# Optimization experiments

Measured on AMD Instinct MI355X. Metric: run time of the kernel, lower is better.

Reference implementation:

```python
import jax, jax.numpy as jnp
import numpy as np

BT = 64  # chunk size

def _l2norm(x, eps=1e-6):
    n = jnp.linalg.norm(x, axis=-1, keepdims=True)
    return x / jnp.maximum(n, eps)

def _kda_gate(g_raw, A_log, dt_bias):
    # g = -exp(A_log) * softplus(g_raw + dt_bias); broadcast A_log over K
    return -jnp.exp(A_log)[None, None, :, None] * jax.nn.softplus(g_raw.astype(jnp.float32) + dt_bias[None, None].astype(jnp.float32))

def _chunk_kda_fwd(q, k, v, g, beta):
    B, T, H, K = q.shape
    V = v.shape[-1]
    assert T % BT == 0
    NT = T // BT
    scale = K ** -0.5
    q = _l2norm(q.astype(jnp.float32)) * scale
    k = _l2norm(k.astype(jnp.float32))

    def to_chunks(x, d):
        # [B,T,H,d] -> [NT,B,H,BT,d]
        return x.astype(jnp.float32).transpose(0, 2, 1, 3).reshape(B, H, NT, BT, d).transpose(2, 0, 1, 3, 4)

    qc, kc, vc, gc = to_chunks(q, K), to_chunks(k, K), to_chunks(v, V), to_chunks(g, K)
    bc = beta.astype(jnp.float32).transpose(0, 2, 1).reshape(B, H, NT, BT).transpose(2, 0, 1, 3)  # [NT,B,H,BT]

    eye = jnp.eye(BT, dtype=jnp.float32)
    tril_strict = jnp.tril(jnp.ones((BT, BT), bool), -1)
    tril_incl = jnp.tril(jnp.ones((BT, BT), bool), 0)

    def body(S, xs):
        q_i, k_i, v_i, g_i, b_i = xs  # [B,H,BT,*]
        gcum = jnp.cumsum(g_i, axis=-2)                              # [B,H,BT,K]
        diff = gcum[:, :, :, None, :] - gcum[:, :, None, :, :]      # [B,H,BT,BT,K]
        decay = jnp.exp(jnp.minimum(diff, 0.0))
        # intra-chunk k-k matrix, beta row-scaled, strictly lower, negated
        Akk = jnp.einsum('bhik,bhjk,bhijk->bhij', k_i, k_i, decay)
        M = -jnp.where(tril_strict, Akk * b_i[..., :, None], 0.0)
        # UT transform: torch in-place loop solves Tm = (I - M)^{-1}
        Tm = jax.scipy.linalg.solve_triangular(eye - M, jnp.broadcast_to(eye, M.shape), lower=True)
        Afin = Tm * b_i[..., None, :]                                # column scale by beta
        k_eg = k_i * jnp.exp(gcum)
        w = Afin @ k_eg                                              # [B,H,BT,K]
        u = Afin @ v_i                                               # [B,H,BT,V]
        Aqk = jnp.einsum('bhik,bhjk,bhijk->bhij', q_i, k_i, decay)
        Aqk = jnp.where(tril_incl, Aqk, 0.0)
        v_new = u - w @ S
        o_i = (q_i * jnp.exp(gcum)) @ S + Aqk @ v_new
        g_last = gcum[:, :, -1, :]                                   # [B,H,K]
        k_dec = jnp.exp(g_last[:, :, None, :] - gcum) * k_i
        S_new = S * jnp.exp(g_last)[..., None] + jnp.einsum('bhck,bhcv->bhkv', k_dec, v_new)
        return S_new, o_i

    S0 = jnp.zeros((B, H, K, V), jnp.float32)
    _, o = jax.lax.scan(body, S0, (qc, kc, vc, gc, bc))              # o: [NT,B,H,BT,V]
    return o.transpose(1, 2, 0, 3, 4).reshape(B, H, T, V).transpose(0, 2, 1, 3)


def setup_inputs() -> dict:
    key = jax.random.key(0)
    ks = jax.random.split(key, 7)
    B, T, H, K, V = 2, 8192, 16, 32, 64
    return {
        'q': jax.random.normal(ks[0], (B, T, H, K), jnp.float32),
        'k': jax.random.normal(ks[1], (B, T, H, K), jnp.float32),
        'v': jax.random.normal(ks[2], (B, T, H, V), jnp.float32),
        'g_raw': jax.random.normal(ks[3], (B, T, H, K), jnp.float32),
        'beta': jax.random.uniform(ks[4], (B, T, H), jnp.float32),
        'A_log': jax.random.normal(ks[5], (H,), jnp.float32) - 3.0,  # moderate decay rate
        'dt_bias': jax.random.normal(ks[6], (H, K), jnp.float32) * 0.1,
    }


def reference(q, k, v, g_raw, beta, A_log, dt_bias):
    g = _kda_gate(g_raw, A_log, dt_bias)
    return _chunk_kda_fwd(q, k, v, g, beta)
```

## Files before the change

### kernel.cpp

```cpp
#include <hip/hip_runtime.h>
#include <math.h>

#define Tt 8192
#define Hh 16
#define NCH 4096

#define OFF_U   ((size_t)NCH*2048)
#define OFF_M   ((size_t)NCH*6144)
#define OFF_C   ((size_t)NCH*7168)
#define OFF_MS  ((size_t)NCH*9216)
#define OFF_CS  (OFF_MS + (size_t)256*1024)
#define OFF_SS  (OFF_CS + (size_t)256*2048)

__device__ __forceinline__ float softplusf(float x) {
  return fmaxf(x, 0.f) + log1pf(__expf(-fabsf(x)));
}

__global__ __launch_bounds__(256) void kda_phase1(
    const float* __restrict__ kin, const float* __restrict__ vin,
    const float* __restrict__ graw, const float* __restrict__ beta,
    const float* __restrict__ A_log, const float* __restrict__ dt_bias,
    float* __restrict__ ws)
{
  __shared__ float sG[64*33];
  __shared__ float sK[64*33];
  __shared__ float sL[64*64];
  __shared__ float sT[64*65];
  __shared__ float sC2[3*272];
  __shared__ float sEgl[32];

  const int tid = threadIdx.x;
  const int ch = blockIdx.x;
  const int c = ch >> 5, bh = ch & 31;
  const int b = bh >> 4, h = bh & 15;
  const int t0 = c*64;
  const int iq = tid >> 2, kq = (tid & 3)*8;

  float* wsW = ws;
  float* wsU = ws + OFF_U;
  float* wsM = ws + OFF_M;
  float* wsCc= ws + OFF_C;

  const float negA = -__expf(A_log[h]);

  {
    const float* gr = graw + (((size_t)b*Tt + t0 + iq)*Hh + h)*32 + kq;
    const float* db = dt_bias + h*32 + kq;
    #pragma unroll
    for (int r = 0; r < 8; ++r)
      sG[iq*33 + kq + r] = negA * softplusf(gr[r] + db[r]);
  }
  __syncthreads();
  if (tid < 32) {
    float acc = 0.f;
    for (int i = 0; i < 64; ++i) { acc += sG[i*33 + tid]; sG[i*33 + tid] = acc; }
  }
  {
    const float* kp = kin + (((size_t)b*Tt + t0 + iq)*Hh + h)*32 + kq;
    float kr[8]; float ss = 0.f;
    #pragma unroll
    for (int r = 0; r < 8; ++r) { kr[r] = kp[r]; ss += kr[r]*kr[r]; }
    ss += __shfl_xor(ss, 1); ss += __shfl_xor(ss, 2);
    const float sc = 1.f / fmaxf(sqrtf(ss), 1e-6f);
    #pragma unroll
    for (int r = 0; r < 8; ++r) sK[iq*33 + kq + r] = kr[r]*sc;
  }
  __syncthreads();

  const float b_cm = beta[((size_t)b*Tt + t0 + (tid & 63))*Hh + h];
  float* P  = sT;
  float* Qb = sT + 2112;
  const int i64 = tid & 63, jj2 = (tid >> 6)*2;
  for (int jt = 0; jt < 8; ++jt) {
    const int j0 = jt*8;
    #pragma unroll
    for (int r = 0; r < 8; ++r) {
      const int idx = iq*33 + kq + r;
      P[idx] = sK[idx] * __expf(fminf(sG[idx] - sG[j0*33 + kq + r], 0.f));
    }
    {
      const int jj = tid >> 5, kk = tid & 31;
      Qb[jj*32 + kk] = sK[(j0+jj)*33 + kk] * __expf(sG[j0*33 + kk] - sG[(j0+jj)*33 + kk]);
    }
    __syncthreads();
    float a0 = 0.f, a1 = 0.f;
    #pragma unroll
    for (int hf = 0; hf < 2; ++hf) {
      const int k0 = hf*16;
      float qa[16], qb[16];
      #pragma unroll
      for (int t4 = 0; t4 < 4; ++t4) {
        float4 xa = *(const float4*)(Qb + (jj2  )*32 + k0 + t4*4);
        float4 xb = *(const float4*)(Qb + (jj2+1)*32 + k0 + t4*4);
        qa[t4*4+0]=xa.x; qa[t4*4+1]=xa.y; qa[t4*4+2]=xa.z; qa[t4*4+3]=xa.w;
        qb[t4*4+0]=xb.x; qb[t4*4+1]=xb.y; qb[t4*4+2]=xb.z; qb[t4*4+3]=xb.w;
      }
      #pragma unroll
      for (int kk = 0; kk < 16; ++kk) {
        const float p = P[i64*33 + k0 + kk];
        a0 += p * qa[kk]; a1 += p * qb[kk];
      }
    }
    const int j_0 = j0 + jj2;
    sL[(j_0  )*64 + i64] = (i64 > j_0  ) ? a0*b_cm : 0.f;
    sL[(j_0+1)*64 + i64] = (i64 > j_0+1) ? a1*b_cm : 0.f;
    __syncthreads();
  }

  for (int e = tid; e < 4096; e += 256) {
    const int row = e >> 6, col = e & 63;
    sT[row*65 + col] = (row == col) ? 1.f : 0.f;
  }
  __syncthreads();
  if (tid < 64) {
    const int p = tid >> 4, col = tid & 15;
    for (int i = 1; i < 16; ++i) {
      const int gi = p*16 + i, gc = p*16 + col;
      float acc = 0.f;
      for (int j = 0; j < i; ++j)
        acc -= sL[(p*16+j)*64 + gi] * sT[(p*16+j)*65 + gc];
      sT[gi*65 + gc] = acc + ((i == col) ? 1.f : 0.f);
    }
  }
  __syncthreads();
  {
    const int wid = tid >> 6;
    const int lane = tid & 63;
    const int ri = lane & 15, c4 = (lane >> 4)*4;
    auto offblk = [&](int p, int q) {
      float a0=0.f, a1=0.f, a2=0.f, a3=0.f;
      for (int m = q; m < p; ++m) {
        #pragma unroll
        for (int j = 0; j < 16; ++j) {
          const float lv = sL[(m*16+j)*64 + p*16+ri];
          const float* tp = sT + (m*16+j)*65 + q*16 + c4;
          a0 += lv*tp[0]; a1 += lv*tp[1]; a2 += lv*tp[2]; a3 += lv*tp[3];
        }
      }
      float* cp = sC2 + wid*272 + ri*17 + c4;
      cp[0]=a0; cp[1]=a1; cp[2]=a2; cp[3]=a3;
      float b0=0.f, b1=0.f, b2=0.f, b3=0.f;
      #pragma unroll
      for (int j = 0; j < 16; ++j) {
        const float tv = sT[(p*16+ri)*65 + p*16 + j];
        const float* cj = sC2 + wid*272 + j*17 + c4;
        b0 += tv*cj[0]; b1 += tv*cj[1]; b2 += tv*cj[2]; b3 += tv*cj[3];
      }
      float* op = sT + (p*16+ri)*65 + q*16 + c4;
      op[0]=-b0; op[1]=-b1; op[2]=-b2; op[3]=-b3;
    };
    if (wid == 0) offblk(1,0); else if (wid == 1) offblk(2,1); else if (wid == 2) offblk(3,2);
    __syncthreads();
    if (wid == 0) offblk(2,0); else if (wid == 1) offblk(3,1);
    __syncthreads();
    if (wid == 0) offblk(3,0);
  }
  __syncthreads();

  {
    const float b_row = beta[((size_t)b*Tt + t0 + iq)*Hh + h];
    #pragma unroll
    for (int r = 0; r < 8; ++r) {
      const int idx = iq*33 + kq + r;
      const float g = sG[idx], kn = sK[idx];
      sL[iq*32 + kq + r] = b_row * kn * __expf(g);
      sK[idx] = kn * __expf(sG[63*33 + kq + r] - g);
    }
    if (tid < 32) sEgl[tid] = __expf(sG[63*33 + tid]);
  }
  __syncthreads();

  {
    float acc[8] = {0,0,0,0,0,0,0,0};
    for (int j = 0; j <= iq; ++j) {
      const float t = sT[iq*65 + j];
      const float4 e0 = *(const float4*)(sL + j*32 + kq);
      const float4 e1 = *(const float4*)(sL + j*32 + kq + 4);
      acc[0]+=t*e0.x; acc[1]+=t*e0.y; acc[2]+=t*e0.z; acc[3]+=t*e0.w;
      acc[4]+=t*e1.x; acc[5]+=t*e1.y; acc[6]+=t*e1.z; acc[7]+=t*e1.w;
    }
    #pragma unroll
    for (int r = 0; r < 8; ++r) {
      wsW[(size_t)ch*2048 + tid*8 + r] = acc[r];
      sG[iq*32 + kq + r] = acc[r];
    }
  }
  __syncthreads();

  {
    #pragma unroll
    for (int r = 0; r < 4; ++r) {
      const int f = tid + 256*r;
      const int j = f >> 4, qd = f & 15;
      const float bj = beta[((size_t)b*Tt + t0 + j)*Hh + h];
      float4 v4 = *(const float4*)(vin + (((size_t)b*Tt + t0 + j)*Hh + h)*64 + qd*4);
      v4.x *= bj; v4.y *= bj; v4.z *= bj; v4.w *= bj;
      *(float4*)(sL + j*64 + qd*4) = v4;
    }
  }
  __syncthreads();

  float uacc[16];
  {
    const int vs = (tid & 3)*16;
    #pragma unroll
    for (int r = 0; r < 16; ++r) uacc[r] = 0.f;
    for (int j = 0; j <= iq; ++j) {
      const float t = sT[iq*65 + j];
      const float4 e0 = *(const float4*)(sL + j*64 + vs);
      const float4 e1 = *(const float4*)(sL + j*64 + vs + 4);
      const float4 e2 = *(const float4*)(sL + j*64 + vs + 8);
      const float4 e3 = *(const float4*)(sL + j*64 + vs + 12);
      uacc[0]+=t*e0.x;  uacc[1]+=t*e0.y;  uacc[2]+=t*e0.z;  uacc[3]+=t*e0.w;
      uacc[4]+=t*e1.x;  uacc[5]+=t*e1.y;  uacc[6]+=t*e1.z;  uacc[7]+=t*e1.w;
      uacc[8]+=t*e2.x;  uacc[9]+=t*e2.y;  uacc[10]+=t*e2.z; uacc[11]+=t*e2.w;
      uacc[12]+=t*e3.x; uacc[13]+=t*e3.y; uacc[14]+=t*e3.z; uacc[15]+=t*e3.w;
    }
    #pragma unroll
    for (int rr = 0; rr < 4; ++rr) {
      float4 o4; o4.x=uacc[rr*4]; o4.y=uacc[rr*4+1]; o4.z=uacc[rr*4+2]; o4.w=uacc[rr*4+3];
      *(float4*)(wsU + (size_t)ch*4096 + tid*16 + rr*4) = o4;
    }
  }
  __syncthreads();
  {
    const int vs = (tid & 3)*16;
    #pragma unroll
    for (int rr = 0; rr < 4; ++rr) {
      float4 o4; o4.x=uacc[rr*4]; o4.y=uacc[rr*4+1]; o4.z=uacc[rr*4+2]; o4.w=uacc[rr*4+3];
      *(float4*)(sL + iq*64 + vs + rr*4) = o4;
    }
  }
  __syncthreads();

  {
    const int a = tid >> 3, b4 = (tid & 7)*4, v8 = (tid & 7)*8;
    float mA[4] = {0,0,0,0};
    float cA[8] = {0,0,0,0,0,0,0,0};
    for (int t = 0; t < 64; ++t) {
      const float kd = sK[t*33 + a];
      const float4 wv = *(const float4*)(sG + t*32 + b4);
      mA[0]+=kd*wv.x; mA[1]+=kd*wv.y; mA[2]+=kd*wv.z; mA[3]+=kd*wv.w;
      const float4 u0 = *(const float4*)(sL + t*64 + v8);
      const float4 u1 = *(const float4*)(sL + t*64 + v8 + 4);
      cA[0]+=kd*u0.x; cA[1]+=kd*u0.y; cA[2]+=kd*u0.z; cA[3]+=kd*u0.w;
      cA[4]+=kd*u1.x; cA[5]+=kd*u1.y; cA[6]+=kd*u1.z; cA[7]+=kd*u1.w;
    }
    float4 m4;
    m4.x = ((a == b4+0) ? sEgl[a] : 0.f) - mA[0];
    m4.y = ((a == b4+1) ? sEgl[a] : 0.f) - mA[1];
    m4.z = ((a == b4+2) ? sEgl[a] : 0.f) - mA[2];
    m4.w = ((a == b4+3) ? sEgl[a] : 0.f) - mA[3];
    *(float4*)(wsM + (size_t)ch*1024 + tid*4) = m4;
    float4 c0, c1;
    c0.x=cA[0]; c0.y=cA[1]; c0.z=cA[2]; c0.w=cA[3];
    c1.x=cA[4]; c1.y=cA[5]; c1.z=cA[6]; c1.w=cA[7];
    *(float4*)(wsCc + (size_t)ch*2048 + tid*8) = c0;
    *(float4*)(wsCc + (size_t)ch*2048 + tid*8 + 4) = c1;
  }
}

__global__ __launch_bounds__(256) void kda_scanA(float* __restrict__ ws)
{
  __shared__ float sMa[32*33];
  __shared__ float sMc[32*33];
  __shared__ float sCa[32*18];
  const int tid = threadIdx.x;
  const int vt = blockIdx.x & 3, seg = (blockIdx.x >> 2) & 7, bh = blockIdx.x >> 5;
  const int v0 = vt*16;
  const int a = tid >> 3, b4 = (tid & 7)*4, c2 = (tid & 7)*2;
  const float* wsM = ws + OFF_M;
  const float* wsC = ws + OFF_C;

  #pragma unroll
  for (int r = 0; r < 4; ++r) sMa[a*33 + b4 + r] = (a == b4 + r) ? 1.f : 0.f;
  sCa[a*18 + c2] = 0.f; sCa[a*18 + c2 + 1] = 0.f;
  __syncthreads();

  for (int i = 0; i < 16; ++i) {
    const int ch = (seg*16 + i)*32 + bh;
    float4 m4 = *(const float4*)(wsM + (size_t)ch*1024 + tid*4);
    float2 cc = *(const float2*)(wsC + (size_t)ch*2048 + a*64 + v0 + c2);
    sMc[a*33+b4+0]=m4.x; sMc[a*33+b4+1]=m4.y; sMc[a*33+b4+2]=m4.z; sMc[a*33+b4+3]=m4.w;
    __syncthreads();
    float cn0 = cc.x, cn1 = cc.y;
    float mn0=0.f, mn1=0.f, mn2=0.f, mn3=0.f;
    for (int bb = 0; bb < 32; ++bb) {
      const float m = sMc[a*33 + bb];
      const float2 s2 = *(const float2*)(sCa + bb*18 + c2);
      cn0 += m*s2.x; cn1 += m*s2.y;
      mn0 += m*sMa[bb*33+b4+0]; mn1 += m*sMa[bb*33+b4+1];
      mn2 += m*sMa[bb*33+b4+2]; mn3 += m*sMa[bb*33+b4+3];
    }
    __syncthreads();
    sCa[a*18+c2] = cn0; sCa[a*18+c2+1] = cn1;
    sMa[a*33+b4+0]=mn0; sMa[a*33+b4+1]=mn1; sMa[a*33+b4+2]=mn2; sMa[a*33+b4+3]=mn3;
    __syncthreads();
  }
  const size_t sid = (size_t)(bh*8 + seg);
  float* wsMs = ws + OFF_MS;
  float* wsCs = ws + OFF_CS;
  if (vt == 0) {
    #pragma unroll
    for (int r = 0; r < 4; ++r) wsMs[sid*1024 + tid*4 + r] = sMa[a*33+b4+r];
  }
  float2 co; co.x = sCa[a*18+c2]; co.y = sCa[a*18+c2+1];
  *(float2*)(wsCs + sid*2048 + a*64 + v0 + c2) = co;
}

__global__ __launch_bounds__(256) void kda_scanB(float* __restrict__ ws)
{
  __shared__ float sS[32*64];
  __shared__ float sM[32*33];
  __shared__ float sC2[32*64];
  const int tid = threadIdx.x;
  const int bh = blockIdx.x;
  const int a = tid >> 3, b4 = (tid & 7)*4, v8 = (tid & 7)*8;
  const float* wsMs = ws + OFF_MS;
  const float* wsCs = ws + OFF_CS;
  float* wsSs = ws + OFF_SS;

  #pragma unroll
  for (int r = 0; r < 8; ++r) sS[a*64 + v8 + r] = 0.f;
  __syncthreads();
  for (int seg = 0; seg < 8; ++seg) {
    const size_t sid = (size_t)(bh*8 + seg);
    #pragma unroll
    for (int r = 0; r < 8; ++r) wsSs[sid*2048 + tid*8 + r] = sS[a*64+v8+r];
    float4 m4 = *(const float4*)(wsMs + sid*1024 + tid*4);
    float4 c0 = *(const float4*)(wsCs + sid*2048 + tid*8);
    float4 c1 = *(const float4*)(wsCs + sid*2048 + tid*8 + 4);
    sM[a*33+b4+0]=m4.x; sM[a*33+b4+1]=m4.y; sM[a*33+b4+2]=m4.z; sM[a*33+b4+3]=m4.w;
    sC2[a*64+v8+0]=c0.x; sC2[a*64+v8+1]=c0.y; sC2[a*64+v8+2]=c0.z; sC2[a*64+v8+3]=c0.w;
    sC2[a*64+v8+4]=c1.x; sC2[a*64+v8+5]=c1.y; sC2[a*64+v8+6]=c1.z; sC2[a*64+v8+7]=c1.w;
    __syncthreads();
    float n0=0,n1=0,n2=0,n3=0,n4=0,n5=0,n6=0,n7=0;
    for (int bb = 0; bb < 32; ++bb) {
      const float m = sM[a*33 + bb];
      const float4 s0 = *(const float4*)(sS + bb*64 + v8);
      const float4 s1 = *(const float4*)(sS + bb*64 + v8 + 4);
      n0 += m*s0.x; n1 += m*s0.y; n2 += m*s0.z; n3 += m*s0.w;
      n4 += m*s1.x; n5 += m*s1.y; n6 += m*s1.z; n7 += m*s1.w;
    }
    n0 += sC2[a*64+v8+0]; n1 += sC2[a*64+v8+1]; n2 += sC2[a*64+v8+2]; n3 += sC2[a*64+v8+3];
    n4 += sC2[a*64+v8+4]; n5 += sC2[a*64+v8+5]; n6 += sC2[a*64+v8+6]; n7 += sC2[a*64+v8+7];
    __syncthreads();
    sS[a*64+v8+0]=n0; sS[a*64+v8+1]=n1; sS[a*64+v8+2]=n2; sS[a*64+v8+3]=n3;
    sS[a*64+v8+4]=n4; sS[a*64+v8+5]=n5; sS[a*64+v8+6]=n6; sS[a*64+v8+7]=n7;
    __syncthreads();
  }
}

__global__ __launch_bounds__(256) void kda_scanC(float* __restrict__ ws)
{
  __shared__ float sM[32*33];
  __shared__ float sS[32*18];
  const int tid = threadIdx.x;
  const int vt = blockIdx.x & 3, seg = (blockIdx.x >> 2) & 7, bh = blockIdx.x >> 5;
  const int v0 = vt*16;
  const int a = tid >> 3, b4 = (tid & 7)*4, c2 = (tid & 7)*2;
  const float* wsM = ws + OFF_M;
  float* wsC = ws + OFF_C;
  const float* wsSs = ws + OFF_SS;

  const size_t sid = (size_t)(bh*8 + seg);
  {
    float2 s0 = *(const float2*)(wsSs + sid*2048 + a*64 + v0 + c2);
    sS[a*18 + c2] = s0.x; sS[a*18 + c2 + 1] = s0.y;
  }
  __syncthreads();

  for (int i = 0; i < 16; ++i) {
    const int ch = (seg*16 + i)*32 + bh;
    float4 m4 = *(const float4*)(wsM + (size_t)ch*1024 + tid*4);
    float2 cc = *(const float2*)(wsC + (size_t)ch*2048 + a*64 + v0 + c2);
    sM[a*33+b4+0]=m4.x; sM[a*33+b4+1]=m4.y; sM[a*33+b4+2]=m4.z; sM[a*33+b4+3]=m4.w;
    float2 se; se.x = sS[a*18+c2]; se.y = sS[a*18+c2+1];
    *(float2*)(wsC + (size_t)ch*2048 + a*64 + v0 + c2) = se;
    __syncthreads();
    float n0 = cc.x, n1 = cc.y;
    for (int bb = 0; bb < 32; ++bb) {
      const float m = sM[a*33 + bb];
      const float2 s2 = *(const float2*)(sS + bb*18 + c2);
      n0 += m*s2.x; n1 += m*s2.y;
    }
    __syncthreads();
    sS[a*18+c2] = n0; sS[a*18+c2+1] = n1;
    __syncthreads();
  }
}

__global__ __launch_bounds__(256) void kda_phase3(
    const float* __restrict__ qin, const float* __restrict__ kin,
    const float* __restrict__ graw,
    const float* __restrict__ A_log, const float* __restrict__ dt_bias,
    const float* __restrict__ ws, float* __restrict__ out)
{
  __shared__ float sG[64*33];
  __shared__ float sQ[64*33];
  __shared__ float sA[64*65];
  __shared__ float sV[64*64];

  const int tid = threadIdx.x;
  const int ch = blockIdx.x;
  const int c = ch >> 5, bh = ch & 31;
  const int b = bh >> 4, h = bh & 15;
  const int t0 = c*64;
  const int iq = tid >> 2, kq = (tid & 3)*8;

  const float* wsW = ws;
  const float* wsU = ws + OFF_U;
  const float* wsS = ws + OFF_C;

  const float negA = -__expf(A_log[h]);
  {
    const float* gr = graw + (((size_t)b*Tt + t0 + iq)*Hh + h)*32 + kq;
    const float* db = dt_bias + h*32 + kq;
    #pragma unroll
    for (int r = 0; r < 8; ++r)
      sG[iq*33 + kq + r] = negA * softplusf(gr[r] + db[r]);
  }
  __syncthreads();
  if (tid < 32) {
    float acc = 0.f;
    for (int i = 0; i < 64; ++i) { acc += sG[i*33 + tid]; sG[i*33 + tid] = acc; }
  }
  float knr[8];
  {
    const float* qp = qin + (((size_t)b*Tt + t0 + iq)*Hh + h)*32 + kq;
    float qr[8]; float ssq = 0.f;
    #pragma unroll
    for (int r = 0; r < 8; ++r) { qr[r] = qp[r]; ssq += qr[r]*qr[r]; }
    ssq += __shfl_xor(ssq, 1); ssq += __shfl_xor(ssq, 2);
    const float scq = 0.17677669529663687f / fmaxf(sqrtf(ssq), 1e-6f);
    #pragma unroll
    for (int r = 0; r < 8; ++r) sQ[iq*33 + kq + r] = qr[r]*scq;

    const float* kp = kin + (((size_t)b*Tt + t0 + iq)*Hh + h)*32 + kq;
    float ssk = 0.f;
    #pragma unroll
    for (int r = 0; r < 8; ++r) { knr[r] = kp[r]; ssk += knr[r]*knr[r]; }
    ssk += __shfl_xor(ssk, 1); ssk += __shfl_xor(ssk, 2);
    const float sck = 1.f / fmaxf(sqrtf(ssk), 1e-6f);
    #pragma unroll
    for (int r = 0; r < 8; ++r) knr[r] *= sck;
  }
  __syncthreads();

  float* P  = sV;
  float* Qb = sV + 2112;
  const int i64 = tid & 63, jj2 = (tid >> 6)*2;
  for (int jt = 0; jt < 8; ++jt) {
    const int j0 = jt*8;
    #pragma unroll
    for (int r = 0; r < 8; ++r) {
      const int idx = iq*33 + kq + r;
      P[idx] = sQ[idx] * __expf(fminf(sG[idx] - sG[j0*33 + kq + r], 0.f));
    }
    if (iq >= j0 && iq < j0 + 8) {
      const int jj = iq - j0;
      #pragma unroll
      for (int r = 0; r < 8; ++r)
        Qb[jj*32 + kq + r] = knr[r] * __expf(sG[j0*33 + kq + r] - sG[iq*33 + kq + r]);
    }
    __syncthreads();
    float a0 = 0.f, a1 = 0.f;
    #pragma unroll
    for (int hf = 0; hf < 2; ++hf) {
      const int k0 = hf*16;
      float qa[16], qb[16];
      #pragma unroll
      for (int t4 = 0; t4 < 4; ++t4) {
        float4 xa = *(const float4*)(Qb + (jj2  )*32 + k0 + t4*4);
        float4 xb = *(const float4*)(Qb + (jj2+1)*32 + k0 + t4*4);
        qa[t4*4+0]=xa.x; qa[t4*4+1]=xa.y; qa[t4*4+2]=xa.z; qa[t4*4+3]=xa.w;
        qb[t4*4+0]=xb.x; qb[t4*4+1]=xb.y; qb[t4*4+2]=xb.z; qb[t4*4+3]=xb.w;
      }
      #pragma unroll
      for (int kk = 0; kk < 16; ++kk) {
        const float p = P[i64*33 + k0 + kk];
        a0 += p * qa[kk]; a1 += p * qb[kk];
      }
    }
    const int j_0 = j0 + jj2;
    sA[i64*65 + j_0  ] = (i64 >= j_0  ) ? a0 : 0.f;
    sA[i64*65 + j_0+1] = (i64 >= j_0+1) ? a1 : 0.f;
    __syncthreads();
  }

  float qgr[8];
  {
    #pragma unroll
    for (int r = 0; r < 8; ++r) {
      const int idx = iq*33 + kq + r;
      qgr[r] = sQ[idx] * __expf(sG[idx]);
    }
  }
  __syncthreads();
  {
    #pragma unroll
    for (int rr = 0; rr < 2; ++rr) {
      const int f = tid + 256*rr;
      *(float4*)(sG + f*4) = *(const float4*)(wsS + (size_t)ch*2048 + f*4);
    }
    *(float4*)(sV + tid*8)     = *(const float4*)(wsW + (size_t)ch*2048 + tid*8);
    *(float4*)(sV + tid*8 + 4) = *(const float4*)(wsW + (size_t)ch*2048 + tid*8 + 4);
  }
  __syncthreads();
  {
    float qe[8];
    #pragma unroll
    for (int r = 0; r < 8; ++r) qe[r] = qgr[r];
    for (int j = 0; j <= iq; ++j) {
      const float av = sA[iq*65 + j];
      const float4 w0 = *(const float4*)(sV + j*32 + kq);
      const float4 w1 = *(const float4*)(sV + j*32 + kq + 4);
      qe[0]-=av*w0.x; qe[1]-=av*w0.y; qe[2]-=av*w0.z; qe[3]-=av*w0.w;
      qe[4]-=av*w1.x; qe[5]-=av*w1.y; qe[6]-=av*w1.z; qe[7]-=av*w1.w;
    }
    #pragma unroll
    for (int r = 0; r < 8; ++r) sQ[iq*33 + kq + r] = qe[r];
  }
  __syncthreads();
  {
    #pragma unroll
    for (int rr = 0; rr < 4; ++rr) {
      const int f = tid + 256*rr;
      *(float4*)(sV + f*4) = *(const float4*)(wsU + (size_t)ch*4096 + f*4);
    }
  }
  __syncthreads();
  {
    const int vs = (tid & 3)*16;
    float acc[16];
    #pragma unroll
    for (int r = 0; r < 16; ++r) acc[r] = 0.f;
    for (int kk = 0; kk < 32; ++kk) {
      const float qv = sQ[iq*33 + kk];
      const float4 s0 = *(const float4*)(sG + kk*64 + vs);
      const float4 s1 = *(const float4*)(sG + kk*64 + vs + 4);
      const float4 s2 = *(const float4*)(sG + kk*64 + vs + 8);
      const float4 s3 = *(const float4*)(sG + kk*64 + vs + 12);
      acc[0]+=qv*s0.x;  acc[1]+=qv*s0.y;  acc[2]+=qv*s0.z;  acc[3]+=qv*s0.w;
      acc[4]+=qv*s1.x;  acc[5]+=qv*s1.y;  acc[6]+=qv*s1.z;  acc[7]+=qv*s1.w;
      acc[8]+=qv*s2.x;  acc[9]+=qv*s2.y;  acc[10]+=qv*s2.z; acc[11]+=qv*s2.w;
      acc[12]+=qv*s3.x; acc[13]+=qv*s3.y; acc[14]+=qv*s3.z; acc[15]+=qv*s3.w;
    }
    for (int j = 0; j <= iq; ++j) {
      const float av = sA[iq*65 + j];
      const float4 u0 = *(const float4*)(sV + j*64 + vs);
      const float4 u1 = *(const float4*)(sV + j*64 + vs + 4);
      const float4 u2 = *(const float4*)(sV + j*64 + vs + 8);
      const float4 u3 = *(const float4*)(sV + j*64 + vs + 12);
      acc[0]+=av*u0.x;  acc[1]+=av*u0.y;  acc[2]+=av*u0.z;  acc[3]+=av*u0.w;
      acc[4]+=av*u1.x;  acc[5]+=av*u1.y;  acc[6]+=av*u1.z;  acc[7]+=av*u1.w;
      acc[8]+=av*u2.x;  acc[9]+=av*u2.y;  acc[10]+=av*u2.z; acc[11]+=av*u2.w;
      acc[12]+=av*u3.x; acc[13]+=av*u3.y; acc[14]+=av*u3.z; acc[15]+=av*u3.w;
    }
    float* op = out + (((size_t)b*Tt + t0 + iq)*Hh + h)*64 + vs;
    #pragma unroll
    for (int rr = 0; rr < 4; ++rr) {
      float4 o4; o4.x=acc[rr*4]; o4.y=acc[rr*4+1]; o4.z=acc[rr*4+2]; o4.w=acc[rr*4+3];
      *(float4*)(op + rr*4) = o4;
    }
  }
}

extern "C" void kernel_launch(void* const* d_in, const int* in_sizes, int n_in,
                              void* d_out, int out_size, void* d_ws, size_t ws_size,
                              hipStream_t stream) {
  const float* q    = (const float*)d_in[0];
  const float* k    = (const float*)d_in[1];
  const float* v    = (const float*)d_in[2];
  const float* graw = (const float*)d_in[3];
  const float* beta = (const float*)d_in[4];
  const float* A_log= (const float*)d_in[5];
  const float* dtb  = (const float*)d_in[6];
  float* out = (float*)d_out;
  float* ws  = (float*)d_ws;

  kda_phase1<<<NCH, 256, 0, stream>>>(k, v, graw, beta, A_log, dtb, ws);
  kda_scanA<<<1024, 256, 0, stream>>>(ws);
  kda_scanB<<<32, 256, 0, stream>>>(ws);
  kda_scanC<<<1024, 256, 0, stream>>>(ws);
  kda_phase3<<<NCH, 256, 0, stream>>>(q, k, graw, A_log, dtb, ws, out);
}
```

Measured before the change: 572.6 us.

## Double block size for chunk kernels, split scanB over V, prefetch scan loads

Phase1 and phase3 move from 256 to 512 threads per chunk, so each thread handles 4 K-elements instead of 8. The intra-chunk loops, the block-triangular inverse (now two 256-thread groups) and the state-update products are re-indexed to match. scanB is split across V tiles to run on 128 blocks instead of 32. scanA, scanB and scanC now prefetch the next chunk's M/C from global memory and drop one barrier per iteration. The aim is more parallelism and latency hiding, at the cost of more barriers per thread and heavier per-block shared-memory occupancy.

```diff
diff --git a/kernel.cpp b/kernel.cpp
--- a/kernel.cpp
+++ b/kernel.cpp
@@ -16,7 +16,7 @@
   return fmaxf(x, 0.f) + log1pf(__expf(-fabsf(x)));
 }
 
-__global__ __launch_bounds__(256) void kda_phase1(
+__global__ __launch_bounds__(512, 6) void kda_phase1(
     const float* __restrict__ kin, const float* __restrict__ vin,
     const float* __restrict__ graw, const float* __restrict__ beta,
     const float* __restrict__ A_log, const float* __restrict__ dt_bias,
@@ -26,7 +26,7 @@
   __shared__ float sK[64*33];
   __shared__ float sL[64*64];
   __shared__ float sT[64*65];
-  __shared__ float sC2[3*272];
+  __shared__ float sC2[2*272];
   __shared__ float sEgl[32];
 
   const int tid = threadIdx.x;
@@ -34,7 +34,7 @@
   const int c = ch >> 5, bh = ch & 31;
   const int b = bh >> 4, h = bh & 15;
   const int t0 = c*64;
-  const int iq = tid >> 2, kq = (tid & 3)*8;
+  const int iq = tid >> 3, kq = (tid & 7)*4;
 
   float* wsW = ws;
   float* wsU = ws + OFF_U;
@@ -47,23 +47,29 @@
     const float* gr = graw + (((size_t)b*Tt + t0 + iq)*Hh + h)*32 + kq;
     const float* db = dt_bias + h*32 + kq;
     #pragma unroll
-    for (int r = 0; r < 8; ++r)
+    for (int r = 0; r < 4; ++r)
       sG[iq*33 + kq + r] = negA * softplusf(gr[r] + db[r]);
   }
   __syncthreads();
   if (tid < 32) {
-    float acc = 0.f;
-    for (int i = 0; i < 64; ++i) { acc += sG[i*33 + tid]; sG[i*33 + tid] = acc; }
+    float c0 = 0.f;
+    for (int blk = 0; blk < 4; ++blk) {
+      float v[16];
+      #pragma unroll
+      for (int i = 0; i < 16; ++i) v[i] = sG[(blk*16+i)*33 + tid];
+      #pragma unroll
+      for (int i = 0; i < 16; ++i) { c0 += v[i]; sG[(blk*16+i)*33 + tid] = c0; }
+    }
   }
   {
     const float* kp = kin + (((size_t)b*Tt + t0 + iq)*Hh + h)*32 + kq;
-    float kr[8]; float ss = 0.f;
-    #pragma unroll
-    for (int r = 0; r < 8; ++r) { kr[r] = kp[r]; ss += kr[r]*kr[r]; }
-    ss += __shfl_xor(ss, 1); ss += __shfl_xor(ss, 2);
+    float kr[4]; float ss = 0.f;
+    #pragma unroll
+    for (int r = 0; r < 4; ++r) { kr[r] = kp[r]; ss += kr[r]*kr[r]; }
+    ss += __shfl_xor(ss, 1); ss += __shfl_xor(ss, 2); ss += __shfl_xor(ss, 4);
     const float sc = 1.f / fmaxf(sqrtf(ss), 1e-6f);
     #pragma unroll
-    for (int r = 0; r < 8; ++r) sK[iq*33 + kq + r] = kr[r]*sc;
+    for (int r = 0; r < 4; ++r) sK[iq*33 + kq + r] = kr[r]*sc;
   }
   __syncthreads();
 
@@ -71,10 +77,10 @@
   float* P  = sT;
   float* Qb = sT + 2112;
   const int i64 = tid & 63, jj2 = (tid >> 6)*2;
-  for (int jt = 0; jt < 8; ++jt) {
-    const int j0 = jt*8;
-    #pragma unroll
-    for (int r = 0; r < 8; ++r) {
+  for (int jt = 0; jt < 4; ++jt) {
+    const int j0 = jt*16;
+    #pragma unroll
+    for (int r = 0; r < 4; ++r) {
       const int idx = iq*33 + kq + r;
       P[idx] = sK[idx] * __expf(fminf(sG[idx] - sG[j0*33 + kq + r], 0.f));
     }
@@ -84,19 +90,18 @@
     }
     __syncthreads();
     float a0 = 0.f, a1 = 0.f;
-    #pragma unroll
-    for (int hf = 0; hf < 2; ++hf) {
-      const int k0 = hf*16;
-      float qa[16], qb[16];
-      #pragma unroll
-      for (int t4 = 0; t4 < 4; ++t4) {
+    for (int k8 = 0; k8 < 4; ++k8) {
+      const int k0 = k8*8;
+      float qa[8], qb[8];
+      #pragma unroll
+      for (int t4 = 0; t4 < 2; ++t4) {
         float4 xa = *(const float4*)(Qb + (jj2  )*32 + k0 + t4*4);
         float4 xb = *(const float4*)(Qb + (jj2+1)*32 + k0 + t4*4);
         qa[t4*4+0]=xa.x; qa[t4*4+1]=xa.y; qa[t4*4+2]=xa.z; qa[t4*4+3]=xa.w;
         qb[t4*4+0]=xb.x; qb[t4*4+1]=xb.y; qb[t4*4+2]=xb.z; qb[t4*4+3]=xb.w;
       }
       #pragma unroll
-      for (int kk = 0; kk < 16; ++kk) {
+      for (int kk = 0; kk < 8; ++kk) {
         const float p = P[i64*33 + k0 + kk];
         a0 += p * qa[kk]; a1 += p * qb[kk];
       }
@@ -107,7 +112,7 @@
     __syncthreads();
   }
 
-  for (int e = tid; e < 4096; e += 256) {
+  for (int e = tid; e < 4096; e += 512) {
     const int row = e >> 6, col = e & 63;
     sT[row*65 + col] = (row == col) ? 1.f : 0.f;
   }
@@ -124,43 +129,36 @@
   }
   __syncthreads();
   {
-    const int wid = tid >> 6;
-    const int lane = tid & 63;
-    const int ri = lane & 15, c4 = (lane >> 4)*4;
-    auto offblk = [&](int p, int q) {
-      float a0=0.f, a1=0.f, a2=0.f, a3=0.f;
+    const int grp = tid >> 8, gl = tid & 255;
+    const int ri = gl & 15, cc = gl >> 4;
+    auto offblk1 = [&](int p, int q) {
+      float acc = 0.f;
       for (int m = q; m < p; ++m) {
         #pragma unroll
-        for (int j = 0; j < 16; ++j) {
-          const float lv = sL[(m*16+j)*64 + p*16+ri];
-          const float* tp = sT + (m*16+j)*65 + q*16 + c4;
-          a0 += lv*tp[0]; a1 += lv*tp[1]; a2 += lv*tp[2]; a3 += lv*tp[3];
-        }
+        for (int j = 0; j < 16; ++j)
+          acc += sL[(m*16+j)*64 + p*16+ri] * sT[(m*16+j)*65 + q*16+cc];
       }
-      float* cp = sC2 + wid*272 + ri*17 + c4;
-      cp[0]=a0; cp[1]=a1; cp[2]=a2; cp[3]=a3;
-      float b0=0.f, b1=0.f, b2=0.f, b3=0.f;
-      #pragma unroll
-      for (int j = 0; j < 16; ++j) {
-        const float tv = sT[(p*16+ri)*65 + p*16 + j];
-        const float* cj = sC2 + wid*272 + j*17 + c4;
-        b0 += tv*cj[0]; b1 += tv*cj[1]; b2 += tv*cj[2]; b3 += tv*cj[3];
-      }
-      float* op = sT + (p*16+ri)*65 + q*16 + c4;
-      op[0]=-b0; op[1]=-b1; op[2]=-b2; op[3]=-b3;
+      sC2[grp*272 + ri*17 + cc] = acc;
     };
-    if (wid == 0) offblk(1,0); else if (wid == 1) offblk(2,1); else if (wid == 2) offblk(3,2);
-    __syncthreads();
-    if (wid == 0) offblk(2,0); else if (wid == 1) offblk(3,1);
-    __syncthreads();
-    if (wid == 0) offblk(3,0);
-  }
-  __syncthreads();
+    auto offblk2 = [&](int p, int q) {
+      float bacc = 0.f;
+      #pragma unroll
+      for (int j = 0; j < 16; ++j)
+        bacc += sT[(p*16+ri)*65 + p*16 + j] * sC2[grp*272 + j*17 + cc];
+      sT[(p*16+ri)*65 + q*16+cc] = -bacc;
+    };
+    int p = grp ? 2 : 1, q = grp ? 1 : 0;
+    offblk1(p,q); __syncthreads(); offblk2(p,q); __syncthreads();
+    p = grp ? 3 : 2; q = grp ? 2 : 0;
+    offblk1(p,q); __syncthreads(); offblk2(p,q); __syncthreads();
+    p = 3; q = grp ? 1 : 0;
+    offblk1(p,q); __syncthreads(); offblk2(p,q); __syncthreads();
+  }
 
   {
     const float b_row = beta[((size_t)b*Tt + t0 + iq)*Hh + h];
     #pragma unroll
-    for (int r = 0; r < 8; ++r) {
+    for (int r = 0; r < 4; ++r) {
       const int idx = iq*33 + kq + r;
       const float g = sG[idx], kn = sK[idx];
       sL[iq*32 + kq + r] = b_row * kn * __expf(g);
@@ -171,26 +169,22 @@
   __syncthreads();
 
   {
-    float acc[8] = {0,0,0,0,0,0,0,0};
+    float acc[4] = {0.f,0.f,0.f,0.f};
     for (int j = 0; j <= iq; ++j) {
       const float t = sT[iq*65 + j];
       const float4 e0 = *(const float4*)(sL + j*32 + kq);
-      const float4 e1 = *(const float4*)(sL + j*32 + kq + 4);
       acc[0]+=t*e0.x; acc[1]+=t*e0.y; acc[2]+=t*e0.z; acc[3]+=t*e0.w;
-      acc[4]+=t*e1.x; acc[5]+=t*e1.y; acc[6]+=t*e1.z; acc[7]+=t*e1.w;
-    }
-    #pragma unroll
-    for (int r = 0; r < 8; ++r) {
-      wsW[(size_t)ch*2048 + tid*8 + r] = acc[r];
-      sG[iq*32 + kq + r] = acc[r];
-    }
-  }
-  __syncthreads();
-
-  {
-    #pragma unroll
-    for (int r = 0; r < 4; ++r) {
-      const int f = tid + 256*r;
+    }
+    float4 o4; o4.x=acc[0]; o4.y=acc[1]; o4.z=acc[2]; o4.w=acc[3];
+    *(float4*)(wsW + (size_t)ch*2048 + tid*4) = o4;
+    *(float4*)(sG + tid*4) = o4;
+  }
+  __syncthreads();
+
+  {
+    #pragma unroll
+    for (int r = 0; r < 2; ++r) {
+      const int f = tid + 512*r;
       const int j = f >> 4, qd = f & 15;
       const float bj = beta[((size_t)b*Tt + t0 + j)*Hh + h];
       float4 v4 = *(const float4*)(vin + (((size_t)b*Tt + t0 + j)*Hh + h)*64 + qd*4);
@@ -200,33 +194,29 @@
   }
   __syncthreads();
 
-  float uacc[16];
-  {
-    const int vs = (tid & 3)*16;
-    #pragma unroll
-    for (int r = 0; r < 16; ++r) uacc[r] = 0.f;
+  float uacc[8];
+  {
+    const int vs = (tid & 7)*8;
+    #pragma unroll
+    for (int r = 0; r < 8; ++r) uacc[r] = 0.f;
     for (int j = 0; j <= iq; ++j) {
       const float t = sT[iq*65 + j];
       const float4 e0 = *(const float4*)(sL + j*64 + vs);
       const float4 e1 = *(const float4*)(sL + j*64 + vs + 4);
-      const float4 e2 = *(const float4*)(sL + j*64 + vs + 8);
-      const float4 e3 = *(const float4*)(sL + j*64 + vs + 12);
-      uacc[0]+=t*e0.x;  uacc[1]+=t*e0.y;  uacc[2]+=t*e0.z;  uacc[3]+=t*e0.w;
-      uacc[4]+=t*e1.x;  uacc[5]+=t*e1.y;  uacc[6]+=t*e1.z;  uacc[7]+=t*e1.w;
-      uacc[8]+=t*e2.x;  uacc[9]+=t*e2.y;  uacc[10]+=t*e2.z; uacc[11]+=t*e2.w;
-      uacc[12]+=t*e3.x; uacc[13]+=t*e3.y; uacc[14]+=t*e3.z; uacc[15]+=t*e3.w;
-    }
-    #pragma unroll
-    for (int rr = 0; rr < 4; ++rr) {
+      uacc[0]+=t*e0.x; uacc[1]+=t*e0.y; uacc[2]+=t*e0.z; uacc[3]+=t*e0.w;
+      uacc[4]+=t*e1.x; uacc[5]+=t*e1.y; uacc[6]+=t*e1.z; uacc[7]+=t*e1.w;
+    }
+    #pragma unroll
+    for (int rr = 0; rr < 2; ++rr) {
       float4 o4; o4.x=uacc[rr*4]; o4.y=uacc[rr*4+1]; o4.z=uacc[rr*4+2]; o4.w=uacc[rr*4+3];
-      *(float4*)(wsU + (size_t)ch*4096 + tid*16 + rr*4) = o4;
-    }
-  }
-  __syncthreads();
-  {
-    const int vs = (tid & 3)*16;
-    #pragma unroll
-    for (int rr = 0; rr < 4; ++rr) {
+      *(float4*)(wsU + (size_t)ch*4096 + tid*8 + rr*4) = o4;
+    }
+  }
+  __syncthreads();
+  {
+    const int vs = (tid & 7)*8;
+    #pragma unroll
+    for (int rr = 0; rr < 2; ++rr) {
       float4 o4; o4.x=uacc[rr*4]; o4.y=uacc[rr*4+1]; o4.z=uacc[rr*4+2]; o4.w=uacc[rr*4+3];
       *(float4*)(sL + iq*64 + vs + rr*4) = o4;
     }
@@ -234,29 +224,22 @@
   __syncthreads();
 
   {
-    const int a = tid >> 3, b4 = (tid & 7)*4, v8 = (tid & 7)*8;
-    float mA[4] = {0,0,0,0};
-    float cA[8] = {0,0,0,0,0,0,0,0};
+    const int a = tid >> 4, b2 = (tid & 15)*2, v4 = (tid & 15)*4;
+    float mA[2] = {0.f, 0.f};
+    float cA[4] = {0.f, 0.f, 0.f, 0.f};
     for (int t = 0; t < 64; ++t) {
       const float kd = sK[t*33 + a];
-      const float4 wv = *(const float4*)(sG + t*32 + b4);
-      mA[0]+=kd*wv.x; mA[1]+=kd*wv.y; mA[2]+=kd*wv.z; mA[3]+=kd*wv.w;
-      const float4 u0 = *(const float4*)(sL + t*64 + v8);
-      const float4 u1 = *(const float4*)(sL + t*64 + v8 + 4);
+      const float2 wv = *(const float2*)(sG + t*32 + b2);
+      mA[0]+=kd*wv.x; mA[1]+=kd*wv.y;
+      const float4 u0 = *(const float4*)(sL + t*64 + v4);
       cA[0]+=kd*u0.x; cA[1]+=kd*u0.y; cA[2]+=kd*u0.z; cA[3]+=kd*u0.w;
-      cA[4]+=kd*u1.x; cA[5]+=kd*u1.y; cA[6]+=kd*u1.z; cA[7]+=kd*u1.w;
-    }
-    float4 m4;
-    m4.x = ((a == b4+0) ? sEgl[a] : 0.f) - mA[0];
-    m4.y = ((a == b4+1) ? sEgl[a] : 0.f) - mA[1];
-    m4.z = ((a == b4+2) ? sEgl[a] : 0.f) - mA[2];
-    m4.w = ((a == b4+3) ? sEgl[a] : 0.f) - mA[3];
-    *(float4*)(wsM + (size_t)ch*1024 + tid*4) = m4;
-    float4 c0, c1;
-    c0.x=cA[0]; c0.y=cA[1]; c0.z=cA[2]; c0.w=cA[3];
-    c1.x=cA[4]; c1.y=cA[5]; c1.z=cA[6]; c1.w=cA[7];
-    *(float4*)(wsCc + (size_t)ch*2048 + tid*8) = c0;
-    *(float4*)(wsCc + (size_t)ch*2048 + tid*8 + 4) = c1;
+    }
+    float2 m2;
+    m2.x = ((a == b2  ) ? sEgl[a] : 0.f) - mA[0];
+    m2.y = ((a == b2+1) ? sEgl[a] : 0.f) - mA[1];
+    *(float2*)(wsM + (size_t)ch*1024 + tid*2) = m2;
+    float4 c4; c4.x=cA[0]; c4.y=cA[1]; c4.z=cA[2]; c4.w=cA[3];
+    *(float4*)(wsCc + (size_t)ch*2048 + tid*4) = c4;
   }
 }
 
@@ -275,14 +258,20 @@
   #pragma unroll
   for (int r = 0; r < 4; ++r) sMa[a*33 + b4 + r] = (a == b4 + r) ? 1.f : 0.f;
   sCa[a*18 + c2] = 0.f; sCa[a*18 + c2 + 1] = 0.f;
-  __syncthreads();
+
+  int ch = (seg*16)*32 + bh;
+  float4 m4 = *(const float4*)(wsM + (size_t)ch*1024 + tid*4);
+  float2 cc = *(const float2*)(wsC + (size_t)ch*2048 + a*64 + v0 + c2);
 
   for (int i = 0; i < 16; ++i) {
-    const int ch = (seg*16 + i)*32 + bh;
-    float4 m4 = *(const float4*)(wsM + (size_t)ch*1024 + tid*4);
-    float2 cc = *(const float2*)(wsC + (size_t)ch*2048 + a*64 + v0 + c2);
     sMc[a*33+b4+0]=m4.x; sMc[a*33+b4+1]=m4.y; sMc[a*33+b4+2]=m4.z; sMc[a*33+b4+3]=m4.w;
     __syncthreads();
+    float4 m4n = m4; float2 ccn = cc;
+    if (i < 15) {
+      const int chn = (seg*16 + i + 1)*32 + bh;
+      m4n = *(const float4*)(wsM + (size_t)chn*1024 + tid*4);
+      ccn = *(const float2*)(wsC + (size_t)chn*2048 + a*64 + v0 + c2);
+    }
     float cn0 = cc.x, cn1 = cc.y;
     float mn0=0.f, mn1=0.f, mn2=0.f, mn3=0.f;
     for (int bb = 0; bb < 32; ++bb) {
@@ -295,7 +284,7 @@
     __syncthreads();
     sCa[a*18+c2] = cn0; sCa[a*18+c2+1] = cn1;
     sMa[a*33+b4+0]=mn0; sMa[a*33+b4+1]=mn1; sMa[a*33+b4+2]=mn2; sMa[a*33+b4+3]=mn3;
-    __syncthreads();
+    m4 = m4n; cc = ccn;
   }
   const size_t sid = (size_t)(bh*8 + seg);
   float* wsMs = ws + OFF_MS;
@@ -310,44 +299,42 @@
 
 __global__ __launch_bounds__(256) void kda_scanB(float* __restrict__ ws)
 {
-  __shared__ float sS[32*64];
+  __shared__ float sS[32*18];
   __shared__ float sM[32*33];
-  __shared__ float sC2[32*64];
   const int tid = threadIdx.x;
-  const int bh = blockIdx.x;
-  const int a = tid >> 3, b4 = (tid & 7)*4, v8 = (tid & 7)*8;
+  const int vt = blockIdx.x & 3, bh = blockIdx.x >> 2;
+  const int v0 = vt*16;
+  const int a = tid >> 3, b4 = (tid & 7)*4, c2 = (tid & 7)*2;
   const float* wsMs = ws + OFF_MS;
   const float* wsCs = ws + OFF_CS;
   float* wsSs = ws + OFF_SS;
 
-  #pragma unroll
-  for (int r = 0; r < 8; ++r) sS[a*64 + v8 + r] = 0.f;
-  __syncthreads();
+  float s0 = 0.f, s1 = 0.f;
+  sS[a*18 + c2] = 0.f; sS[a*18 + c2 + 1] = 0.f;
+  const size_t sid0 = (size_t)(bh*8);
+  float4 m4 = *(const float4*)(wsMs + sid0*1024 + tid*4);
+  float2 cc = *(const float2*)(wsCs + sid0*2048 + a*64 + v0 + c2);
+
   for (int seg = 0; seg < 8; ++seg) {
     const size_t sid = (size_t)(bh*8 + seg);
-    #pragma unroll
-    for (int r = 0; r < 8; ++r) wsSs[sid*2048 + tid*8 + r] = sS[a*64+v8+r];
-    float4 m4 = *(const float4*)(wsMs + sid*1024 + tid*4);
-    float4 c0 = *(const float4*)(wsCs + sid*2048 + tid*8);
-    float4 c1 = *(const float4*)(wsCs + sid*2048 + tid*8 + 4);
+    *(float2*)(wsSs + sid*2048 + a*64 + v0 + c2) = make_float2(s0, s1);
     sM[a*33+b4+0]=m4.x; sM[a*33+b4+1]=m4.y; sM[a*33+b4+2]=m4.z; sM[a*33+b4+3]=m4.w;
-    sC2[a*64+v8+0]=c0.x; sC2[a*64+v8+1]=c0.y; sC2[a*64+v8+2]=c0.z; sC2[a*64+v8+3]=c0.w;
-    sC2[a*64+v8+4]=c1.x; sC2[a*64+v8+5]=c1.y; sC2[a*64+v8+6]=c1.z; sC2[a*64+v8+7]=c1.w;
-    __syncthreads();
-    float n0=0,n1=0,n2=0,n3=0,n4=0,n5=0,n6=0,n7=0;
+    __syncthreads();
+    float4 m4n = m4; float2 ccn = cc;
+    if (seg < 7) {
+      m4n = *(const float4*)(wsMs + (sid+1)*1024 + tid*4);
+      ccn = *(const float2*)(wsCs + (sid+1)*2048 + a*64 + v0 + c2);
+    }
+    float n0 = cc.x, n1 = cc.y;
     for (int bb = 0; bb < 32; ++bb) {
       const float m = sM[a*33 + bb];
-      const float4 s0 = *(const float4*)(sS + bb*64 + v8);
-      const float4 s1 = *(const float4*)(sS + bb*64 + v8 + 4);
-      n0 += m*s0.x; n1 += m*s0.y; n2 += m*s0.z; n3 += m*s0.w;
-      n4 += m*s1.x; n5 += m*s1.y; n6 += m*s1.z; n7 += m*s1.w;
-    }
-    n0 += sC2[a*64+v8+0]; n1 += sC2[a*64+v8+1]; n2 += sC2[a*64+v8+2]; n3 += sC2[a*64+v8+3];
-    n4 += sC2[a*64+v8+4]; n5 += sC2[a*64+v8+5]; n6 += sC2[a*64+v8+6]; n7 += sC2[a*64+v8+7];
-    __syncthreads();
-    sS[a*64+v8+0]=n0; sS[a*64+v8+1]=n1; sS[a*64+v8+2]=n2; sS[a*64+v8+3]=n3;
-    sS[a*64+v8+4]=n4; sS[a*64+v8+5]=n5; sS[a*64+v8+6]=n6; sS[a*64+v8+7]=n7;
-    __syncthreads();
+      const float2 s2 = *(const float2*)(sS + bb*18 + c2);
+      n0 += m*s2.x; n1 += m*s2.y;
+    }
+    __syncthreads();
+    s0 = n0; s1 = n1;
+    sS[a*18+c2] = s0; sS[a*18+c2+1] = s1;
+    m4 = m4n; cc = ccn;
   }
 }
 
@@ -364,20 +351,27 @@
   const float* wsSs = ws + OFF_SS;
 
   const size_t sid = (size_t)(bh*8 + seg);
-  {
-    float2 s0 = *(const float2*)(wsSs + sid*2048 + a*64 + v0 + c2);
-    sS[a*18 + c2] = s0.x; sS[a*18 + c2 + 1] = s0.y;
-  }
-  __syncthreads();
+  float s0, s1;
+  {
+    float2 sv = *(const float2*)(wsSs + sid*2048 + a*64 + v0 + c2);
+    s0 = sv.x; s1 = sv.y;
+    sS[a*18 + c2] = s0; sS[a*18 + c2 + 1] = s1;
+  }
+  int ch = (seg*16)*32 + bh;
+  float4 m4 = *(const float4*)(wsM + (size_t)ch*1024 + tid*4);
+  float2 cc = *(const float2*)(wsC + (size_t)ch*2048 + a*64 + v0 + c2);
 
   for (int i = 0; i < 16; ++i) {
-    const int ch = (seg*16 + i)*32 + bh;
-    float4 m4 = *(const float4*)(wsM + (size_t)ch*1024 + tid*4);
-    float2 cc = *(const float2*)(wsC + (size_t)ch*2048 + a*64 + v0 + c2);
+    const int chc = (seg*16 + i)*32 + bh;
     sM[a*33+b4+0]=m4.x; sM[a*33+b4+1]=m4.y; sM[a*33+b4+2]=m4.z; sM[a*33+b4+3]=m4.w;
-    float2 se; se.x = sS[a*18+c2]; se.y = sS[a*18+c2+1];
-    *(float2*)(wsC + (size_t)ch*2048 + a*64 + v0 + c2) = se;
-    __syncthreads();
+    *(float2*)(wsC + (size_t)chc*2048 + a*64 + v0 + c2) = make_float2(s0, s1);
+    __syncthreads();
+    float4 m4n = m4; float2 ccn = cc;
+    if (i < 15) {
+      const int chn = (seg*16 + i + 1)*32 + bh;
+      m4n = *(const float4*)(wsM + (size_t)chn*1024 + tid*4);
+      ccn = *(const float2*)(wsC + (size_t)chn*2048 + a*64 + v0 + c2);
+    }
     float n0 = cc.x, n1 = cc.y;
     for (int bb = 0; bb < 32; ++bb) {
       const float m = sM[a*33 + bb];
@@ -385,12 +379,13 @@
       n0 += m*s2.x; n1 += m*s2.y;
     }
     __syncthreads();
-    sS[a*18+c2] = n0; sS[a*18+c2+1] = n1;
-    __syncthreads();
-  }
-}
-
-__global__ __launch_bounds__(256) void kda_phase3(
+    s0 = n0; s1 = n1;
+    sS[a*18+c2] = s0; sS[a*18+c2+1] = s1;
+    m4 = m4n; cc = ccn;
+  }
+}
+
+__global__ __launch_bounds__(512, 6) void kda_phase3(
     const float* __restrict__ qin, const float* __restrict__ kin,
     const float* __restrict__ graw,
     const float* __restrict__ A_log, const float* __restrict__ dt_bias,
@@ -406,7 +401,7 @@
   const int c = ch >> 5, bh = ch & 31;
   const int b = bh >> 4, h = bh & 15;
   const int t0 = c*64;
-  const int iq = tid >> 2, kq = (tid & 3)*8;
+  const int iq = tid >> 3, kq = (tid & 7)*4;
 
   const float* wsW = ws;
   const float* wsU = ws + OFF_U;
@@ -417,67 +412,72 @@
     const float* gr = graw + (((size_t)b*Tt + t0 + iq)*Hh + h)*32 + kq;
     const float* db = dt_bias + h*32 + kq;
     #pragma unroll
-    for (int r = 0; r < 8; ++r)
+    for (int r = 0; r < 4; ++r)
       sG[iq*33 + kq + r] = negA * softplusf(gr[r] + db[r]);
   }
   __syncthreads();
   if (tid < 32) {
-    float acc = 0.f;
-    for (int i = 0; i < 64; ++i) { acc += sG[i*33 + tid]; sG[i*33 + tid] = acc; }
-  }
-  float knr[8];
+    float c0 = 0.f;
+    for (int blk = 0; blk < 4; ++blk) {
+      float v[16];
+      #pragma unroll
+      for (int i = 0; i < 16; ++i) v[i] = sG[(blk*16+i)*33 + tid];
+      #pragma unroll
+      for (int i = 0; i < 16; ++i) { c0 += v[i]; sG[(blk*16+i)*33 + tid] = c0; }
+    }
+  }
+  float knr[4];
   {
     const float* qp = qin + (((size_t)b*Tt + t0 + iq)*Hh + h)*32 + kq;
-    float qr[8]; float ssq = 0.f;
-    #pragma unroll
-    for (int r = 0; r < 8; ++r) { qr[r] = qp[r]; ssq += qr[r]*qr[r]; }
-    ssq += __shfl_xor(ssq, 1); ssq += __shfl_xor(ssq, 2);
+    float qr[4]; float ssq = 0.f;
+    #pragma unroll
+    for (int r = 0; r < 4; ++r) { qr[r] = qp[r]; ssq += qr[r]*qr[r]; }
+    ssq += __shfl_xor(ssq, 1); ssq += __shfl_xor(ssq, 2); ssq += __shfl_xor(ssq, 4);
     const float scq = 0.17677669529663687f / fmaxf(sqrtf(ssq), 1e-6f);
     #pragma unroll
-    for (int r = 0; r < 8; ++r) sQ[iq*33 + kq + r] = qr[r]*scq;
+    for (int r = 0; r < 4; ++r) sQ[iq*33 + kq + r] = qr[r]*scq;
 
     const float* kp = kin + (((size_t)b*Tt + t0 + iq)*Hh + h)*32 + kq;
     float ssk = 0.f;
     #pragma unroll
-    for (int r = 0; r < 8; ++r) { knr[r] = kp[r]; ssk += knr[r]*knr[r]; }
-    ssk += __shfl_xor(ssk, 1); ssk += __shfl_xor(ssk, 2);
+    for (int r = 0; r < 4; ++r) { knr[r] = kp[r]; ssk += knr[r]*knr[r]; }
+    ssk += __shfl_xor(ssk, 1); ssk += __shfl_xor(ssk, 2); ssk += __shfl_xor(ssk, 4);
     const float sck = 1.f / fmaxf(sqrtf(ssk), 1e-6f);
     #pragma unroll
-    for (int r = 0; r < 8; ++r) knr[r] *= sck;
+    for (int r = 0; r < 4; ++r) knr[r] *= sck;
   }
   __syncthreads();
 
   float* P  = sV;
   float* Qb = sV + 2112;
   const int i64 = tid & 63, jj2 = (tid >> 6)*2;
-  for (int jt = 0; jt < 8; ++jt) {
-    const int j0 = jt*8;
-    #pragma unroll
-    for (int r = 0; r < 8; ++r) {
+  for (int jt = 0; jt < 4; ++jt) {
+    const int j0 = jt*16;
+    #pragma unroll
+    for (int r = 0; r < 4; ++r) {
       const int idx = iq*33 + kq + r;
       P[idx] = sQ[idx] * __expf(fminf(sG[idx] - sG[j0*33 + kq + r], 0.f));
     }
-    if (iq >= j0 && iq < j0 + 8) {
+    if (iq >= j0 && iq < j0 + 16) {
       const int jj = iq - j0;
       #pragma unroll
-      for (int r = 0; r < 8; ++r)
+      for (int r = 0; r < 4; ++r)
         Qb[jj*32 + kq + r] = knr[r] * __expf(sG[j0*33 + kq + r] - sG[iq*33 + kq + r]);
     }
     __syncthreads();
     float a0 = 0.f, a1 = 0.f;
-    #pragma unroll
-    for (int hf = 0; hf < 2; ++hf) {
-      const int k0 = hf*16;
-      float qa[16], qb[16];
-      #pragma unroll
-      for (int t4 = 0; t4 < 4; ++t4) {
+    for (int k8 = 0; k8 < 4; ++k8) {
+      const int k0 = k8*8;
+      float qa[8], qb[8];
+      #pragma unroll
+      for (int t4 = 0; t4 < 2; ++t4) {
         float4 xa = *(const float4*)(Qb + (jj2  )*32 + k0 + t4*4);
         float4 xb = *(const float4*)(Qb + (jj2+1)*32 + k0 + t4*4);
         qa[t4*4+0]=xa.x; qa[t4*4+1]=xa.y; qa[t4*4+2]=xa.z; qa[t4*4+3]=xa.w;
         qb[t4*4+0]=xb.x; qb[t4*4+1]=xb.y; qb[t4*4+2]=xb.z; qb[t4*4+3]=xb.w;
       }
       #pragma unroll
-      for (int kk = 0; kk < 16; ++kk) {
+      for (int kk = 0; kk < 8; ++kk) {
         const float p = P[i64*33 + k0 + kk];
         a0 += p * qa[kk]; a1 += p * qb[kk];
       }
@@ -488,81 +488,63 @@
     __syncthreads();
   }
 
-  float qgr[8];
-  {
-    #pragma unroll
-    for (int r = 0; r < 8; ++r) {
+  float qgr[4];
+  {
+    #pragma unroll
+    for (int r = 0; r < 4; ++r) {
       const int idx = iq*33 + kq + r;
       qgr[r] = sQ[idx] * __expf(sG[idx]);
     }
   }
   __syncthreads();
   {
-    #pragma unroll
-    for (int rr = 0; rr < 2; ++rr) {
-      const int f = tid + 256*rr;
-      *(float4*)(sG + f*4) = *(const float4*)(wsS + (size_t)ch*2048 + f*4);
-    }
-    *(float4*)(sV + tid*8)     = *(const float4*)(wsW + (size_t)ch*2048 + tid*8);
-    *(float4*)(sV + tid*8 + 4) = *(const float4*)(wsW + (size_t)ch*2048 + tid*8 + 4);
-  }
-  __syncthreads();
-  {
-    float qe[8];
-    #pragma unroll
-    for (int r = 0; r < 8; ++r) qe[r] = qgr[r];
+    *(float4*)(sG + tid*4) = *(const float4*)(wsS + (size_t)ch*2048 + tid*4);
+    *(float4*)(sV + tid*4) = *(const float4*)(wsW + (size_t)ch*2048 + tid*4);
+  }
+  __syncthreads();
+  {
+    float qe[4];
+    #pragma unroll
+    for (int r = 0; r < 4; ++r) qe[r] = qgr[r];
     for (int j = 0; j <= iq; ++j) {
       const float av = sA[iq*65 + j];
       const float4 w0 = *(const float4*)(sV + j*32 + kq);
-      const float4 w1 = *(const float4*)(sV + j*32 + kq + 4);
       qe[0]-=av*w0.x; qe[1]-=av*w0.y; qe[2]-=av*w0.z; qe[3]-=av*w0.w;
-      qe[4]-=av*w1.x; qe[5]-=av*w1.y; qe[6]-=av*w1.z; qe[7]-=av*w1.w;
-    }
-    #pragma unroll
-    for (int r = 0; r < 8; ++r) sQ[iq*33 + kq + r] = qe[r];
-  }
-  __syncthreads();
-  {
-    #pragma unroll
-    for (int rr = 0; rr < 4; ++rr) {
-      const int f = tid + 256*rr;
+    }
+    #pragma unroll
+    for (int r = 0; r < 4; ++r) sQ[iq*33 + kq + r] = qe[r];
+  }
+  __syncthreads();
+  {
+    #pragma unroll
+    for (int rr = 0; rr < 2; ++rr) {
+      const int f = tid + 512*rr;
       *(float4*)(sV + f*4) = *(const float4*)(wsU + (size_t)ch*4096 + f*4);
     }
   }
   __syncthreads();
   {
-    const int vs = (tid & 3)*16;
-    float acc[16];
-    #pragma unroll
-    for (int r = 0; r < 16; ++r) acc[r] = 0.f;
+    const int vs = (tid & 7)*8;
+    float acc[8];
+    #pragma unroll
+    for (int r = 0; r < 8; ++r) acc[r] = 0.f;
     for (int kk = 0; kk < 32; ++kk) {
       const float qv = sQ[iq*33 + kk];
       const float4 s0 = *(const float4*)(sG + kk*64 + vs);
       const float4 s1 = *(const float4*)(sG + kk*64 + vs + 4);
-      const float4 s2 = *(const float4*)(sG + kk*64 + vs + 8);
-      const float4 s3 = *(const float4*)(sG + kk*64 + vs + 12);
-      acc[0]+=qv*s0.x;  acc[1]+=qv*s0.y;  acc[2]+=qv*s0.z;  acc[3]+=qv*s0.w;
-      acc[4]+=qv*s1.x;  acc[5]+=qv*s1.y;  acc[6]+=qv*s1.z;  acc[7]+=qv*s1.w;
-      acc[8]+=qv*s2.x;  acc[9]+=qv*s2.y;  acc[10]+=qv*s2.z; acc[11]+=qv*s2.w;
-      acc[12]+=qv*s3.x; acc[13]+=qv*s3.y; acc[14]+=qv*s3.z; acc[15]+=qv*s3.w;
+      acc[0]+=qv*s0.x; acc[1]+=qv*s0.y; acc[2]+=qv*s0.z; acc[3]+=qv*s0.w;
+      acc[4]+=qv*s1.x; acc[5]+=qv*s1.y; acc[6]+=qv*s1.z; acc[7]+=qv*s1.w;
     }
     for (int j = 0; j <= iq; ++j) {
       const float av = sA[iq*65 + j];
       const float4 u0 = *(const float4*)(sV + j*64 + vs);
       const float4 u1 = *(const float4*)(sV + j*64 + vs + 4);
-      const float4 u2 = *(const float4*)(sV + j*64 + vs + 8);
-      const float4 u3 = *(const float4*)(sV + j*64 + vs + 12);
-      acc[0]+=av*u0.x;  acc[1]+=av*u0.y;  acc[2]+=av*u0.z;  acc[3]+=av*u0.w;
-      acc[4]+=av*u1.x;  acc[5]+=av*u1.y;  acc[6]+=av*u1.z;  acc[7]+=av*u1.w;
-      acc[8]+=av*u2.x;  acc[9]+=av*u2.y;  acc[10]+=av*u2.z; acc[11]+=av*u2.w;
-      acc[12]+=av*u3.x; acc[13]+=av*u3.y; acc[14]+=av*u3.z; acc[15]+=av*u3.w;
+      acc[0]+=av*u0.x; acc[1]+=av*u0.y; acc[2]+=av*u0.z; acc[3]+=av*u0.w;
+      acc[4]+=av*u1.x; acc[5]+=av*u1.y; acc[6]+=av*u1.z; acc[7]+=av*u1.w;
     }
     float* op = out + (((size_t)b*Tt + t0 + iq)*Hh + h)*64 + vs;
-    #pragma unroll
-    for (int rr = 0; rr < 4; ++rr) {
-      float4 o4; o4.x=acc[rr*4]; o4.y=acc[rr*4+1]; o4.z=acc[rr*4+2]; o4.w=acc[rr*4+3];
-      *(float4*)(op + rr*4) = o4;
-    }
+    *(float4*)(op)     = make_float4(acc[0],acc[1],acc[2],acc[3]);
+    *(float4*)(op + 4) = make_float4(acc[4],acc[5],acc[6],acc[7]);
   }
 }
 
@@ -579,9 +561,9 @@
   float* out = (float*)d_out;
   float* ws  = (float*)d_ws;
 
-  kda_phase1<<<NCH, 256, 0, stream>>>(k, v, graw, beta, A_log, dtb, ws);
+  kda_phase1<<<NCH, 512, 0, stream>>>(k, v, graw, beta, A_log, dtb, ws);
   kda_scanA<<<1024, 256, 0, stream>>>(ws);
-  kda_scanB<<<32, 256, 0, stream>>>(ws);
+  kda_scanB<<<128, 256, 0, stream>>>(ws);
   kda_scanC<<<1024, 256, 0, stream>>>(ws);
-  kda_phase3<<<NCH, 256, 0, stream>>>(q, k, graw, A_log, dtb, ws, out);
-}
+  kda_phase3<<<NCH, 512, 0, stream>>>(q, k, graw, A_log, dtb, ws, out);
+}
```

Result: slower. 1.852 ms (+223.3%).
